# Performance work log

Measured on AMD Instinct MI355X. Metric: run time of the kernel, lower is better.

The kernel has to match this reference:

```python
import jax, jax.numpy as jnp
import numpy as np

L = 96
K = 3  # conv kernel size

def setup_inputs() -> dict:
    key = jax.random.key(0)
    ks = jax.random.split(key, 6)
    linear_x = jax.random.randint(ks[0], (4 * L**3,), 0, 2, dtype=jnp.int32)
    tetraeder_2 = jax.random.normal(ks[1], (2, 2), dtype=jnp.float32)
    w1 = jax.random.normal(ks[2], (K, K, K, 12, 16), dtype=jnp.float32) * 0.05
    b1 = jnp.zeros((16,), dtype=jnp.float32)
    w2 = jax.random.normal(ks[3], (K, K, K, 16, 32), dtype=jnp.float32) * 0.05
    b2 = jnp.zeros((32,), dtype=jnp.float32)
    wd = jax.random.normal(ks[4], (32, 1), dtype=jnp.float32) * 0.1
    return {"linear_x": linear_x, "tetraeder_2": tetraeder_2,
            "w1": w1, "b1": b1, "w2": w2, "b2": b2, "wd": wd}

def _bonds(linear_x, tetraeder_2):
    # x: (L,L,L,4) spin config; v: (L,L,L,4,d) per-site vectors via gather
    x = linear_x.reshape(L, L, L, 4)
    v = tetraeder_2[x]
    v0, v1, v2, v3 = v[..., 0, :], v[..., 1, :], v[..., 2, :], v[..., 3, :]
    # roll(v, 1, ax)[a] == v[(a-1) % L] -> periodic neighbor cells cell_1/2/3
    r1 = jnp.roll(v1, 1, axis=0)
    r2 = jnp.roll(v2, 1, axis=1)
    r3 = jnp.roll(v3, 1, axis=2)
    dot = lambda a, b: jnp.einsum('...d,...d->...', a, b)
    # 12 bonds in the exact order of on_unit_cell
    bonds = [dot(v0, v1), dot(v0, v2), dot(v0, v3),
             dot(v0, r1), dot(v0, r2), dot(v0, r3),
             dot(v1, v2), dot(v2, v3), dot(v3, v1),
             dot(r1, r2), dot(r2, r3), dot(r3, r1)]
    return jnp.stack(bonds, axis=-1)  # (L,L,L,12)

def _conv_block(y, w, b):
    pad = [(0, 0)] + [((K - 1) // 2, K // 2)] * 3 + [(0, 0)]
    y = jnp.pad(y, pad, mode='wrap')
    y = jax.lax.conv_general_dilated(
        y, w, window_strides=(1, 1, 1), padding='VALID',
        dimension_numbers=('NDHWC', 'DHWIO', 'NDHWC'))
    return jax.nn.elu(y + b)

def reference(linear_x, tetraeder_2, w1, b1, w2, b2, wd):
    y = _bonds(linear_x, tetraeder_2)[jnp.newaxis, ...]  # (1,L,L,L,12)
    y = _conv_block(y, w1, b1)
    y = _conv_block(y, w2, b2)
    y = jnp.mean(y, axis=(1, 2, 3)).ravel()  # (32,)
    return (y @ wd).ravel()[0]
```

## Files before the change

kernel.cpp:

```cpp
#include <hip/hip_runtime.h>
#include <hip/hip_bf16.h>
#include <cmath>

#define L 96
#define L3 (L*L*L)
#define NT 4
#define NCONV 864
#define BSTRIDE 456

__device__ __constant__ const int TAU[27] = {
    0,16,32, 288,304,320, 576,592,608,
    1728,1744,1760, 2016,2032,2048, 2304,2320,2336,
    3456,3472,3488, 3744,3760,3776, 4032,4048,4064};

typedef __attribute__((ext_vector_type(8))) short short8;
typedef __attribute__((ext_vector_type(4))) float floatx4;

__device__ __forceinline__ float eluf(float x) {
    float e = __expf(x) - 1.0f;
    return x > 0.0f ? x : e;
}

__device__ __forceinline__ unsigned short f2bf(float f) {
    __hip_bfloat16 h = __float2bfloat16(f);
    return *reinterpret_cast<unsigned short*>(&h);
}

__device__ __forceinline__ int wrapc(int x) {
    if (x < 0) x += L;
    if (x >= L) x -= L;
    return x;
}

__global__ __launch_bounds__(256) void prepw_kernel(
    const float* __restrict__ w1, const float* __restrict__ w2,
    unsigned short* __restrict__ Bm1, unsigned short* __restrict__ Bm2)
{
    int idx = blockIdx.x * 256 + threadIdx.x;
    if (idx < 16*BSTRIDE) {
        int o = idx / BSTRIDE, k = idx % BSTRIDE;
        int tau = k >> 4, i = k & 15;
        float v = (k < 448 && tau < 27 && i < 12) ? w1[tau*192 + i*16 + o] : 0.0f;
        Bm1[idx] = f2bf(v);
    }
    int j = idx - 16*BSTRIDE;
    if (j >= 0 && j < 32*BSTRIDE) {
        int o = j / BSTRIDE, k = j % BSTRIDE;
        int tau = k >> 4;
        int i = k & 15;
        float v = (k < 448 && tau < 27) ? w2[tau*512 + i*32 + o] : 0.0f;
        Bm2[j] = f2bf(v);
    }
}

__device__ __forceinline__ void bonds_load(
    const int* __restrict__ lx, int W0, int H0, int D0, int tid,
    int4* sv, int* n1, int* n2, int* n3)
{
    #pragma unroll
    for (int i = 0; i < 3; ++i) {
        int t = tid + i*256;
        if (t < 648) {
            int dd = t / 108, rem = t - dd*108;
            int hh = rem / 18, ww = rem - hh*18;
            int gd = wrapc(D0 + dd - 1);
            int gh = wrapc(H0 + hh - 1);
            int gw = wrapc(W0 + ww - 1);
            int gdm = (gd == 0) ? L-1 : gd-1;
            int ghm = (gh == 0) ? L-1 : gh-1;
            int gwm = (gw == 0) ? L-1 : gw-1;
            sv[i] = *reinterpret_cast<const int4*>(lx + 4*((gd*L + gh)*L + gw));
            n1[i] = lx[4*((gdm*L + gh)*L + gw) + 1];
            n2[i] = lx[4*((gd*L + ghm)*L + gw) + 2];
            n3[i] = lx[4*((gd*L + gh)*L + gwm) + 3];
        }
    }
}

__device__ __forceinline__ void bonds_write(
    unsigned short* __restrict__ tile, int tid,
    float d00, float d01, float d11,
    const int4* sv, const int* n1, const int* n2, const int* n3)
{
    #pragma unroll
    for (int i = 0; i < 3; ++i) {
        int t = tid + i*256;
        if (t < 648) {
            int s0 = sv[i].x, s1 = sv[i].y, s2 = sv[i].z, s3 = sv[i].w;
            int r1 = n1[i], r2 = n2[i], r3 = n3[i];
            auto dot = [&](int a, int b) -> float {
                return (a == b) ? (a ? d11 : d00) : d01;
            };
            union { unsigned short s[16]; int4 q[2]; } u;
            u.s[0]  = f2bf(dot(s0, s1));
            u.s[1]  = f2bf(dot(s0, s2));
            u.s[2]  = f2bf(dot(s0, s3));
            u.s[3]  = f2bf(dot(s0, r1));
            u.s[4]  = f2bf(dot(s0, r2));
            u.s[5]  = f2bf(dot(s0, r3));
            u.s[6]  = f2bf(dot(s1, s2));
            u.s[7]  = f2bf(dot(s2, s3));
            u.s[8]  = f2bf(dot(s3, s1));
            u.s[9]  = f2bf(dot(r1, r2));
            u.s[10] = f2bf(dot(r2, r3));
            u.s[11] = f2bf(dot(r3, r1));
            u.s[12] = 0; u.s[13] = 0; u.s[14] = 0; u.s[15] = 0;
            int4* dst = reinterpret_cast<int4*>(tile + t*16);
            dst[0] = u.q[0];
            dst[1] = u.q[1];
        }
    }
}

__device__ __forceinline__ void stage_tile(
    const unsigned short* __restrict__ x, unsigned short* __restrict__ tile,
    int W0, int H0, int D0, int tid)
{
    #pragma unroll
    for (int i = 0; i < 6; ++i) {
        int t = tid + i*256;
        if (i < 5 || t < 1296) {
            int row = t / 36, off = t - row*36;
            int dd = row / 6, hh = row - dd*6;
            int gd = wrapc(D0 + dd - 1);
            int gh = wrapc(H0 + hh - 1);
            int vox = off >> 1, half = off & 1;
            int gw = wrapc(W0 + vox - 1);
            size_t gi = ((size_t)((gd*L + gh)*L + gw))*16 + half*8;
            __builtin_amdgcn_global_load_lds(
                (const __attribute__((address_space(1))) unsigned int*)(x + gi),
                (__attribute__((address_space(3))) unsigned int*)(tile + t*8),
                16, 0, 0);
        }
    }
}

__device__ __forceinline__ void stage_bmat(
    const unsigned short* __restrict__ Bm, unsigned short* __restrict__ Bls,
    int nxfer, int tid)
{
    #pragma unroll
    for (int i = 0; i < 8; ++i) {
        int t = tid + i*256;
        if (t < nxfer) {
            __builtin_amdgcn_global_load_lds(
                (const __attribute__((address_space(1))) unsigned int*)(Bm + t*8),
                (__attribute__((address_space(3))) unsigned int*)(Bls + t*8),
                16, 0, 0);
        }
    }
}

__device__ __forceinline__ void tile_coords(int& bid, int& W0, int& H0, int& Dz)
{
    bid = (blockIdx.z * 24 + blockIdx.y) * 6 + blockIdx.x;
    int nb = (bid & 7) * 108 + (bid >> 3);
    W0 = (nb % 6) * 16;
    int t1 = nb / 6;
    H0 = (t1 % 24) * 4;
    Dz = t1 / 24;
}

__global__ __launch_bounds__(256, 2) void conv1_kernel(
    const int* __restrict__ lx, const float* __restrict__ tet,
    const unsigned short* __restrict__ Bm,
    const float* __restrict__ bias, unsigned short* __restrict__ y)
{
    __shared__ __attribute__((aligned(16))) unsigned short tile[2][6*6*18*16];
    __shared__ __attribute__((aligned(16))) unsigned short Bls[16*BSTRIDE];
    int tid = threadIdx.x;
    int bid, W0, H0, Dz;
    tile_coords(bid, W0, H0, Dz);

    float t00 = tet[0], t01 = tet[1], t10 = tet[2], t11 = tet[3];
    float d00 = t00*t00 + t01*t01;
    float d01 = t00*t10 + t01*t11;
    float d11 = t10*t10 + t11*t11;

    stage_bmat(Bm, Bls, 912, tid);

    int4 sv[3]; int n1[3], n2[3], n3[3];
    bonds_load(lx, W0, H0, Dz*16, tid, sv, n1, n2, n3);
    bonds_write(tile[0], tid, d00, d01, d11, sv, n1, n2, n3);
    __syncthreads();

    int lane = tid & 63, wave = tid >> 6;
    int laneV = lane & 15, g = lane >> 4;
    int gb = g >> 1;
    int abase = laneV*16 + (g & 1)*8;

    float bch[4];
    #pragma unroll
    for (int r = 0; r < 4; ++r) bch[r] = bias[g*4 + r];

    int moff[4];
    #pragma unroll
    for (int m = 0; m < 4; ++m) {
        int mt = wave*4 + m;
        moff[m] = (((mt >> 2)*6 + (mt & 3))*18)*16;
    }

    for (int t = 0; t < NT; ++t) {
        if (t < NT-1)
            bonds_load(lx, W0, H0, Dz*16 + 4*(t+1), tid, sv, n1, n2, n3);

        const unsigned short* tl = tile[t & 1];

        floatx4 acc[4];
        #pragma unroll
        for (int m = 0; m < 4; ++m) acc[m] = (floatx4)(0.0f);

        short8 aC[4], aN[4], bC, bN;
        {
            int a0 = abase + (gb ? TAU[1] : TAU[0]);
            bC = *reinterpret_cast<const short8*>(&Bls[laneV*BSTRIDE + g*8]);
            #pragma unroll
            for (int m = 0; m < 4; ++m)
                aC[m] = *reinterpret_cast<const short8*>(&tl[moff[m] + a0]);
        }

        #pragma unroll
        for (int kt = 0; kt < 14; ++kt) {
            if (kt < 13) {
                int tev = TAU[2*(kt+1)];
                int tod = TAU[(2*(kt+1)+1 > 26) ? 26 : 2*(kt+1)+1];
                int an = abase + (gb ? tod : tev);
                bN = *reinterpret_cast<const short8*>(&Bls[laneV*BSTRIDE + (kt+1)*32 + g*8]);
                #pragma unroll
                for (int m = 0; m < 4; ++m)
                    aN[m] = *reinterpret_cast<const short8*>(&tl[moff[m] + an]);
            }
            __builtin_amdgcn_s_setprio(1);
            #pragma unroll
            for (int m = 0; m < 4; ++m)
                acc[m] = __builtin_amdgcn_mfma_f32_16x16x32_bf16(bC, aC[m], acc[m], 0, 0, 0);
            __builtin_amdgcn_s_setprio(0);
            if (kt < 13) {
                #pragma unroll
                for (int m = 0; m < 4; ++m) aC[m] = aN[m];
                bC = bN;
            }
        }

        if (t < NT-1)
            bonds_write(tile[(t+1) & 1], tid, d00, d01, d11, sv, n1, n2, n3);

        int D0 = Dz*16 + t*4;
        #pragma unroll
        for (int m = 0; m < 4; ++m) {
            int mt = wave*4 + m;
            int d = D0 + (mt >> 2), h = H0 + (mt & 3);
            int w = W0 + laneV;
            union { unsigned short s[4]; uint2 v; } o;
            #pragma unroll
            for (int r = 0; r < 4; ++r)
                o.s[r] = f2bf(eluf(acc[m][r] + bch[r]));
            *reinterpret_cast<uint2*>(&y[((size_t)((d*L + h)*L + w))*16 + g*4]) = o.v;
        }
        __syncthreads();
    }
}

__global__ __launch_bounds__(256, 2) void conv2_kernel(
    const unsigned short* __restrict__ x, const unsigned short* __restrict__ Bm,
    const float* __restrict__ bias, const float* __restrict__ wd,
    float* __restrict__ partials)
{
    __shared__ __attribute__((aligned(16))) unsigned short tile[2][6*6*18*16];
    __shared__ __attribute__((aligned(16))) unsigned short Bls[32*BSTRIDE];
    __shared__ float red[4];
    int tid = threadIdx.x;
    int bid, W0, H0, Dz;
    tile_coords(bid, W0, H0, Dz);

    stage_bmat(Bm, Bls, 1824, tid);
    stage_tile(x, tile[0], W0, H0, Dz*16, tid);
    __syncthreads();

    int lane = tid & 63, wave = tid >> 6;
    int laneV = lane & 15, g = lane >> 4;
    int gb = g >> 1;
    int abase = laneV*16 + (g & 1)*8;
    float b2a = bias[laneV], b2b = bias[16 + laneV];
    float wda = wd[laneV],  wdb = wd[16 + laneV];

    int moff[4];
    #pragma unroll
    for (int m = 0; m < 4; ++m) {
        int mt = wave*4 + m;
        moff[m] = (((mt >> 2)*6 + (mt & 3))*18)*16;
    }

    float s = 0.0f;

    for (int t = 0; t < NT; ++t) {
        if (t < NT-1)
            stage_tile(x, tile[(t+1) & 1], W0, H0, Dz*16 + 4*(t+1), tid);

        const unsigned short* tl = tile[t & 1];

        floatx4 acc[4][2];
        #pragma unroll
        for (int m = 0; m < 4; ++m) {
            acc[m][0] = (floatx4)(0.0f);
            acc[m][1] = (floatx4)(0.0f);
        }

        short8 aC[4], aN[4], bC0, bC1, bN0, bN1;
        {
            int a0 = abase + (gb ? TAU[1] : TAU[0]);
            bC0 = *reinterpret_cast<const short8*>(&Bls[laneV*BSTRIDE + g*8]);
            bC1 = *reinterpret_cast<const short8*>(&Bls[(16 + laneV)*BSTRIDE + g*8]);
            #pragma unroll
            for (int m = 0; m < 4; ++m)
                aC[m] = *reinterpret_cast<const short8*>(&tl[moff[m] + a0]);
        }

        #pragma unroll
        for (int kt = 0; kt < 14; ++kt) {
            if (kt < 13) {
                int tev = TAU[2*(kt+1)];
                int tod = TAU[(2*(kt+1)+1 > 26) ? 26 : 2*(kt+1)+1];
                int an = abase + (gb ? tod : tev);
                bN0 = *reinterpret_cast<const short8*>(&Bls[laneV*BSTRIDE + (kt+1)*32 + g*8]);
                bN1 = *reinterpret_cast<const short8*>(&Bls[(16 + laneV)*BSTRIDE + (kt+1)*32 + g*8]);
                #pragma unroll
                for (int m = 0; m < 4; ++m)
                    aN[m] = *reinterpret_cast<const short8*>(&tl[moff[m] + an]);
            }
            __builtin_amdgcn_s_setprio(1);
            #pragma unroll
            for (int m = 0; m < 4; ++m) {
                acc[m][0] = __builtin_amdgcn_mfma_f32_16x16x32_bf16(aC[m], bC0, acc[m][0], 0, 0, 0);
                acc[m][1] = __builtin_amdgcn_mfma_f32_16x16x32_bf16(aC[m], bC1, acc[m][1], 0, 0, 0);
            }
            __builtin_amdgcn_s_setprio(0);
            if (kt < 13) {
                #pragma unroll
                for (int m = 0; m < 4; ++m) aC[m] = aN[m];
                bC0 = bN0; bC1 = bN1;
            }
        }

        #pragma unroll
        for (int m = 0; m < 4; ++m) {
            #pragma unroll
            for (int reg = 0; reg < 4; ++reg) {
                s += eluf(acc[m][0][reg] + b2a) * wda;
                s += eluf(acc[m][1][reg] + b2b) * wdb;
            }
        }
        __syncthreads();
    }

    #pragma unroll
    for (int off = 32; off; off >>= 1) s += __shfl_down(s, off);
    if (lane == 0) red[wave] = s;
    __syncthreads();
    if (tid == 0) {
        partials[bid] = red[0] + red[1] + red[2] + red[3];
    }
}

__global__ __launch_bounds__(256) void final_kernel(
    const float* __restrict__ partials, float* __restrict__ out)
{
    float s = 0.0f;
    for (int i = threadIdx.x; i < NCONV; i += 256) s += partials[i];
    #pragma unroll
    for (int off = 32; off; off >>= 1) s += __shfl_down(s, off);
    __shared__ float red[4];
    int lane = threadIdx.x & 63;
    int wv   = threadIdx.x >> 6;
    if (lane == 0) red[wv] = s;
    __syncthreads();
    if (threadIdx.x == 0)
        out[0] = (red[0] + red[1] + red[2] + red[3]) * (1.0f / (float)L3);
}

extern "C" void kernel_launch(void* const* d_in, const int* in_sizes, int n_in,
                              void* d_out, int out_size, void* d_ws, size_t ws_size,
                              hipStream_t stream) {
    const int*   lx  = (const int*)  d_in[0];
    const float* tet = (const float*)d_in[1];
    const float* w1  = (const float*)d_in[2];
    const float* b1  = (const float*)d_in[3];
    const float* w2  = (const float*)d_in[4];
    const float* b2  = (const float*)d_in[5];
    const float* wd  = (const float*)d_in[6];
    float* out = (float*)d_out;

    char* ws = (char*)d_ws;
    const size_t ARR_BYTES = (size_t)L3 * 16 * 2;
    unsigned short* y1   = (unsigned short*)ws;
    unsigned short* Bm1  = (unsigned short*)(ws + ARR_BYTES);
    unsigned short* Bm2  = (unsigned short*)(ws + ARR_BYTES + 16*BSTRIDE*2);
    float* partials      = (float*)         (ws + ARR_BYTES + 48*BSTRIDE*2);

    prepw_kernel<<<86, 256, 0, stream>>>(w1, w2, Bm1, Bm2);
    conv1_kernel<<<dim3(6,24,6), 256, 0, stream>>>(lx, tet, Bm1, b1, y1);
    conv2_kernel<<<dim3(6,24,6), 256, 0, stream>>>(y1, Bm2, b2, wd, partials);
    final_kernel<<<1, 256, 0, stream>>>(partials, out);
}
```

Measured before the change: 160.1 us.

## Single-buffer conv LDS tiles to raise occupancy per CU

Replaces the double-buffered LDS input tile in both conv kernels with a single buffer and raises the launch-bounds minimum blocks per CU (4 for conv1, 3 for conv2). The next tile is now written or staged only after a barrier once compute on the current tile finishes, followed by a second barrier. The aim is to cut LDS use so more blocks fit on a CU and hide latency through occupancy instead of in-block prefetch. The cost is that tile staging is serialized with the MFMA work, there is an extra barrier per step, and the tighter register budget may cause spills.

```diff
diff --git a/kernel.cpp b/kernel.cpp
--- a/kernel.cpp
+++ b/kernel.cpp
@@ -161,12 +161,12 @@
     Dz = t1 / 24;
 }
 
-__global__ __launch_bounds__(256, 2) void conv1_kernel(
+__global__ __launch_bounds__(256, 4) void conv1_kernel(
     const int* __restrict__ lx, const float* __restrict__ tet,
     const unsigned short* __restrict__ Bm,
     const float* __restrict__ bias, unsigned short* __restrict__ y)
 {
-    __shared__ __attribute__((aligned(16))) unsigned short tile[2][6*6*18*16];
+    __shared__ __attribute__((aligned(16))) unsigned short tile[6*6*18*16];
     __shared__ __attribute__((aligned(16))) unsigned short Bls[16*BSTRIDE];
     int tid = threadIdx.x;
     int bid, W0, H0, Dz;
@@ -181,7 +181,7 @@
 
     int4 sv[3]; int n1[3], n2[3], n3[3];
     bonds_load(lx, W0, H0, Dz*16, tid, sv, n1, n2, n3);
-    bonds_write(tile[0], tid, d00, d01, d11, sv, n1, n2, n3);
+    bonds_write(tile, tid, d00, d01, d11, sv, n1, n2, n3);
     __syncthreads();
 
     int lane = tid & 63, wave = tid >> 6;
@@ -204,8 +204,6 @@
         if (t < NT-1)
             bonds_load(lx, W0, H0, Dz*16 + 4*(t+1), tid, sv, n1, n2, n3);
 
-        const unsigned short* tl = tile[t & 1];
-
         floatx4 acc[4];
         #pragma unroll
         for (int m = 0; m < 4; ++m) acc[m] = (floatx4)(0.0f);
@@ -216,7 +214,7 @@
             bC = *reinterpret_cast<const short8*>(&Bls[laneV*BSTRIDE + g*8]);
             #pragma unroll
             for (int m = 0; m < 4; ++m)
-                aC[m] = *reinterpret_cast<const short8*>(&tl[moff[m] + a0]);
+                aC[m] = *reinterpret_cast<const short8*>(&tile[moff[m] + a0]);
         }
 
         #pragma unroll
@@ -228,7 +226,7 @@
                 bN = *reinterpret_cast<const short8*>(&Bls[laneV*BSTRIDE + (kt+1)*32 + g*8]);
                 #pragma unroll
                 for (int m = 0; m < 4; ++m)
-                    aN[m] = *reinterpret_cast<const short8*>(&tl[moff[m] + an]);
+                    aN[m] = *reinterpret_cast<const short8*>(&tile[moff[m] + an]);
             }
             __builtin_amdgcn_s_setprio(1);
             #pragma unroll
@@ -242,9 +240,6 @@
             }
         }
 
-        if (t < NT-1)
-            bonds_write(tile[(t+1) & 1], tid, d00, d01, d11, sv, n1, n2, n3);
-
         int D0 = Dz*16 + t*4;
         #pragma unroll
         for (int m = 0; m < 4; ++m) {
@@ -257,16 +252,21 @@
                 o.s[r] = f2bf(eluf(acc[m][r] + bch[r]));
             *reinterpret_cast<uint2*>(&y[((size_t)((d*L + h)*L + w))*16 + g*4]) = o.v;
         }
-        __syncthreads();
-    }
-}
-
-__global__ __launch_bounds__(256, 2) void conv2_kernel(
+
+        if (t < NT-1) {
+            __syncthreads();
+            bonds_write(tile, tid, d00, d01, d11, sv, n1, n2, n3);
+            __syncthreads();
+        }
+    }
+}
+
+__global__ __launch_bounds__(256, 3) void conv2_kernel(
     const unsigned short* __restrict__ x, const unsigned short* __restrict__ Bm,
     const float* __restrict__ bias, const float* __restrict__ wd,
     float* __restrict__ partials)
 {
-    __shared__ __attribute__((aligned(16))) unsigned short tile[2][6*6*18*16];
+    __shared__ __attribute__((aligned(16))) unsigned short tile[6*6*18*16];
     __shared__ __attribute__((aligned(16))) unsigned short Bls[32*BSTRIDE];
     __shared__ float red[4];
     int tid = threadIdx.x;
@@ -274,7 +274,7 @@
     tile_coords(bid, W0, H0, Dz);
 
     stage_bmat(Bm, Bls, 1824, tid);
-    stage_tile(x, tile[0], W0, H0, Dz*16, tid);
+    stage_tile(x, tile, W0, H0, Dz*16, tid);
     __syncthreads();
 
     int lane = tid & 63, wave = tid >> 6;
@@ -294,11 +294,6 @@
     float s = 0.0f;
 
     for (int t = 0; t < NT; ++t) {
-        if (t < NT-1)
-            stage_tile(x, tile[(t+1) & 1], W0, H0, Dz*16 + 4*(t+1), tid);
-
-        const unsigned short* tl = tile[t & 1];
-
         floatx4 acc[4][2];
         #pragma unroll
         for (int m = 0; m < 4; ++m) {
@@ -313,7 +308,7 @@
             bC1 = *reinterpret_cast<const short8*>(&Bls[(16 + laneV)*BSTRIDE + g*8]);
             #pragma unroll
             for (int m = 0; m < 4; ++m)
-                aC[m] = *reinterpret_cast<const short8*>(&tl[moff[m] + a0]);
+                aC[m] = *reinterpret_cast<const short8*>(&tile[moff[m] + a0]);
         }
 
         #pragma unroll
@@ -326,7 +321,7 @@
                 bN1 = *reinterpret_cast<const short8*>(&Bls[(16 + laneV)*BSTRIDE + (kt+1)*32 + g*8]);
                 #pragma unroll
                 for (int m = 0; m < 4; ++m)
-                    aN[m] = *reinterpret_cast<const short8*>(&tl[moff[m] + an]);
+                    aN[m] = *reinterpret_cast<const short8*>(&tile[moff[m] + an]);
             }
             __builtin_amdgcn_s_setprio(1);
             #pragma unroll
@@ -350,7 +345,12 @@
                 s += eluf(acc[m][1][reg] + b2b) * wdb;
             }
         }
-        __syncthreads();
+
+        if (t < NT-1) {
+            __syncthreads();
+            stage_tile(x, tile, W0, H0, Dz*16 + 4*(t+1), tid);
+            __syncthreads();
+        }
     }
 
     #pragma unroll
```

New measurement: 194.1 us. 21.2% more time.

## Load conv2 operands directly from global memory and pad conv1 LDS tile stride

Applied to the files above, without the earlier changes.

conv2 drops its LDS halo tile and double-buffered staging and has each wave read A operands straight from global/L2 with wrapped coordinates. That removes per-iteration barriers and shrinks LDS enough to raise launch bounds to four blocks per CU. conv1 pads its LDS voxel stride from 16 to 24 shorts to reduce bank conflicts and swaps __syncthreads for a cheaper lgkmcnt wait plus barrier. Both kernels drop the s_setprio hints. The risk is that conv2 now issues many redundant uncached-in-LDS global loads with exposed latency inside the MFMA loop.

```diff
diff --git a/kernel.cpp b/kernel.cpp
--- a/kernel.cpp
+++ b/kernel.cpp
@@ -8,10 +8,10 @@
 #define NCONV 864
 #define BSTRIDE 456
 
-__device__ __constant__ const int TAU[27] = {
-    0,16,32, 288,304,320, 576,592,608,
-    1728,1744,1760, 2016,2032,2048, 2304,2320,2336,
-    3456,3472,3488, 3744,3760,3776, 4032,4048,4064};
+__device__ __constant__ const int TAU48[27] = {
+    0,24,48, 432,456,480, 864,888,912,
+    2592,2616,2640, 3024,3048,3072, 3456,3480,3504,
+    5184,5208,5232, 5616,5640,5664, 6048,6072,6096};
 
 typedef __attribute__((ext_vector_type(8))) short short8;
 typedef __attribute__((ext_vector_type(4))) float floatx4;
@@ -30,6 +30,12 @@
     if (x < 0) x += L;
     if (x >= L) x -= L;
     return x;
+}
+
+__device__ __forceinline__ void lgkm_barrier() {
+    asm volatile("s_waitcnt lgkmcnt(0)" ::: "memory");
+    __builtin_amdgcn_s_barrier();
+    __builtin_amdgcn_sched_barrier(0);
 }
 
 __global__ __launch_bounds__(256) void prepw_kernel(
@@ -105,32 +111,9 @@
             u.s[10] = f2bf(dot(r2, r3));
             u.s[11] = f2bf(dot(r3, r1));
             u.s[12] = 0; u.s[13] = 0; u.s[14] = 0; u.s[15] = 0;
-            int4* dst = reinterpret_cast<int4*>(tile + t*16);
+            int4* dst = reinterpret_cast<int4*>(tile + t*24);
             dst[0] = u.q[0];
             dst[1] = u.q[1];
-        }
-    }
-}
-
-__device__ __forceinline__ void stage_tile(
-    const unsigned short* __restrict__ x, unsigned short* __restrict__ tile,
-    int W0, int H0, int D0, int tid)
-{
-    #pragma unroll
-    for (int i = 0; i < 6; ++i) {
-        int t = tid + i*256;
-        if (i < 5 || t < 1296) {
-            int row = t / 36, off = t - row*36;
-            int dd = row / 6, hh = row - dd*6;
-            int gd = wrapc(D0 + dd - 1);
-            int gh = wrapc(H0 + hh - 1);
-            int vox = off >> 1, half = off & 1;
-            int gw = wrapc(W0 + vox - 1);
-            size_t gi = ((size_t)((gd*L + gh)*L + gw))*16 + half*8;
-            __builtin_amdgcn_global_load_lds(
-                (const __attribute__((address_space(1))) unsigned int*)(x + gi),
-                (__attribute__((address_space(3))) unsigned int*)(tile + t*8),
-                16, 0, 0);
         }
     }
 }
@@ -166,7 +149,7 @@
     const unsigned short* __restrict__ Bm,
     const float* __restrict__ bias, unsigned short* __restrict__ y)
 {
-    __shared__ __attribute__((aligned(16))) unsigned short tile[2][6*6*18*16];
+    __shared__ __attribute__((aligned(16))) unsigned short tile[2][6*6*18*24];
     __shared__ __attribute__((aligned(16))) unsigned short Bls[16*BSTRIDE];
     int tid = threadIdx.x;
     int bid, W0, H0, Dz;
@@ -187,7 +170,7 @@
     int lane = tid & 63, wave = tid >> 6;
     int laneV = lane & 15, g = lane >> 4;
     int gb = g >> 1;
-    int abase = laneV*16 + (g & 1)*8;
+    int abase = laneV*24 + (g & 1)*8;
 
     float bch[4];
     #pragma unroll
@@ -197,7 +180,7 @@
     #pragma unroll
     for (int m = 0; m < 4; ++m) {
         int mt = wave*4 + m;
-        moff[m] = (((mt >> 2)*6 + (mt & 3))*18)*16;
+        moff[m] = ((mt >> 2)*6 + (mt & 3))*432;
     }
 
     for (int t = 0; t < NT; ++t) {
@@ -212,7 +195,7 @@
 
         short8 aC[4], aN[4], bC, bN;
         {
-            int a0 = abase + (gb ? TAU[1] : TAU[0]);
+            int a0 = abase + (gb ? TAU48[1] : TAU48[0]);
             bC = *reinterpret_cast<const short8*>(&Bls[laneV*BSTRIDE + g*8]);
             #pragma unroll
             for (int m = 0; m < 4; ++m)
@@ -222,19 +205,17 @@
         #pragma unroll
         for (int kt = 0; kt < 14; ++kt) {
             if (kt < 13) {
-                int tev = TAU[2*(kt+1)];
-                int tod = TAU[(2*(kt+1)+1 > 26) ? 26 : 2*(kt+1)+1];
+                int tev = TAU48[2*(kt+1)];
+                int tod = TAU48[(2*(kt+1)+1 > 26) ? 26 : 2*(kt+1)+1];
                 int an = abase + (gb ? tod : tev);
                 bN = *reinterpret_cast<const short8*>(&Bls[laneV*BSTRIDE + (kt+1)*32 + g*8]);
                 #pragma unroll
                 for (int m = 0; m < 4; ++m)
                     aN[m] = *reinterpret_cast<const short8*>(&tl[moff[m] + an]);
             }
-            __builtin_amdgcn_s_setprio(1);
             #pragma unroll
             for (int m = 0; m < 4; ++m)
                 acc[m] = __builtin_amdgcn_mfma_f32_16x16x32_bf16(bC, aC[m], acc[m], 0, 0, 0);
-            __builtin_amdgcn_s_setprio(0);
             if (kt < 13) {
                 #pragma unroll
                 for (int m = 0; m < 4; ++m) aC[m] = aN[m];
@@ -257,16 +238,17 @@
                 o.s[r] = f2bf(eluf(acc[m][r] + bch[r]));
             *reinterpret_cast<uint2*>(&y[((size_t)((d*L + h)*L + w))*16 + g*4]) = o.v;
         }
-        __syncthreads();
-    }
-}
-
-__global__ __launch_bounds__(256, 2) void conv2_kernel(
+
+        if (t < NT-1)
+            lgkm_barrier();
+    }
+}
+
+__global__ __launch_bounds__(256, 4) void conv2_kernel(
     const unsigned short* __restrict__ x, const unsigned short* __restrict__ Bm,
     const float* __restrict__ bias, const float* __restrict__ wd,
     float* __restrict__ partials)
 {
-    __shared__ __attribute__((aligned(16))) unsigned short tile[2][6*6*18*16];
     __shared__ __attribute__((aligned(16))) unsigned short Bls[32*BSTRIDE];
     __shared__ float red[4];
     int tid = threadIdx.x;
@@ -274,30 +256,23 @@
     tile_coords(bid, W0, H0, Dz);
 
     stage_bmat(Bm, Bls, 1824, tid);
-    stage_tile(x, tile[0], W0, H0, Dz*16, tid);
     __syncthreads();
 
     int lane = tid & 63, wave = tid >> 6;
     int laneV = lane & 15, g = lane >> 4;
     int gb = g >> 1;
-    int abase = laneV*16 + (g & 1)*8;
     float b2a = bias[laneV], b2b = bias[16 + laneV];
     float wda = wd[laneV],  wdb = wd[16 + laneV];
 
-    int moff[4];
-    #pragma unroll
-    for (int m = 0; m < 4; ++m) {
-        int mt = wave*4 + m;
-        moff[m] = (((mt >> 2)*6 + (mt & 3))*18)*16;
-    }
+    int wb0 = wrapc(W0 + laneV - 1)*16 + (g & 1)*8;
+    int wb1 = wrapc(W0 + laneV    )*16 + (g & 1)*8;
+    int wb2 = wrapc(W0 + laneV + 1)*16 + (g & 1)*8;
 
     float s = 0.0f;
 
     for (int t = 0; t < NT; ++t) {
-        if (t < NT-1)
-            stage_tile(x, tile[(t+1) & 1], W0, H0, Dz*16 + 4*(t+1), tid);
-
-        const unsigned short* tl = tile[t & 1];
+        int D0 = Dz*16 + t*4;
+        int dbase = D0 + wave - 1;
 
         floatx4 acc[4][2];
         #pragma unroll
@@ -307,34 +282,39 @@
         }
 
         short8 aC[4], aN[4], bC0, bC1, bN0, bN1;
-        {
-            int a0 = abase + (gb ? TAU[1] : TAU[0]);
-            bC0 = *reinterpret_cast<const short8*>(&Bls[laneV*BSTRIDE + g*8]);
-            bC1 = *reinterpret_cast<const short8*>(&Bls[(16 + laneV)*BSTRIDE + g*8]);
-            #pragma unroll
-            for (int m = 0; m < 4; ++m)
-                aC[m] = *reinterpret_cast<const short8*>(&tl[moff[m] + a0]);
-        }
+
+        auto loadA = [&](int te, int to, short8* dst) {
+            int kd = gb ? (to/9)     : (te/9);
+            int kh = gb ? ((to/3)%3) : ((te/3)%3);
+            int kwo, kwe = te % 3;  kwo = to % 3;
+            int wsel = gb ? (kwo==0 ? wb0 : (kwo==1 ? wb1 : wb2))
+                          : (kwe==0 ? wb0 : (kwe==1 ? wb1 : wb2));
+            int d = wrapc(dbase + kd);
+            #pragma unroll
+            for (int m = 0; m < 4; ++m) {
+                int h = wrapc(H0 + m - 1 + kh);
+                dst[m] = *reinterpret_cast<const short8*>(&x[(size_t)((d*L + h)*L)*16 + wsel]);
+            }
+        };
+
+        loadA(0, 1, aC);
+        bC0 = *reinterpret_cast<const short8*>(&Bls[laneV*BSTRIDE + g*8]);
+        bC1 = *reinterpret_cast<const short8*>(&Bls[(16 + laneV)*BSTRIDE + g*8]);
 
         #pragma unroll
         for (int kt = 0; kt < 14; ++kt) {
             if (kt < 13) {
-                int tev = TAU[2*(kt+1)];
-                int tod = TAU[(2*(kt+1)+1 > 26) ? 26 : 2*(kt+1)+1];
-                int an = abase + (gb ? tod : tev);
+                int te = 2*(kt+1);
+                int to = (te+1 > 26) ? 26 : te+1;
+                loadA(te, to, aN);
                 bN0 = *reinterpret_cast<const short8*>(&Bls[laneV*BSTRIDE + (kt+1)*32 + g*8]);
                 bN1 = *reinterpret_cast<const short8*>(&Bls[(16 + laneV)*BSTRIDE + (kt+1)*32 + g*8]);
-                #pragma unroll
-                for (int m = 0; m < 4; ++m)
-                    aN[m] = *reinterpret_cast<const short8*>(&tl[moff[m] + an]);
-            }
-            __builtin_amdgcn_s_setprio(1);
+            }
             #pragma unroll
             for (int m = 0; m < 4; ++m) {
                 acc[m][0] = __builtin_amdgcn_mfma_f32_16x16x32_bf16(aC[m], bC0, acc[m][0], 0, 0, 0);
                 acc[m][1] = __builtin_amdgcn_mfma_f32_16x16x32_bf16(aC[m], bC1, acc[m][1], 0, 0, 0);
             }
-            __builtin_amdgcn_s_setprio(0);
             if (kt < 13) {
                 #pragma unroll
                 for (int m = 0; m < 4; ++m) aC[m] = aN[m];
@@ -350,7 +330,6 @@
                 s += eluf(acc[m][1][reg] + b2b) * wdb;
             }
         }
-        __syncthreads();
     }
 
     #pragma unroll
```

New measurement: 255.5 us. 59.6% more time.
